# Kernel tuning notes

Hardware: AMD Instinct MI355X
Metric: run time of the kernel (lower is better)

The kernel has to match this reference:

```python
import jax, jax.numpy as jnp
import numpy as np

DIM = 1024
HEADS = 16
HEAD_DIM = DIM // HEADS
HIDDEN = 4 * DIM
EPS = 1e-5


def _layernorm(x, g, b):
    mu = jnp.mean(x, axis=-1, keepdims=True)
    var = jnp.mean(jnp.square(x - mu), axis=-1, keepdims=True)
    return (x - mu) * jax.lax.rsqrt(var + EPS) * g + b


def setup_inputs() -> dict:
    key = jax.random.key(0)
    ks = jax.random.split(key, 10)
    s = lambda fan_in: 1.0 / np.sqrt(fan_in)
    return {
        "x": jax.random.normal(ks[0], (8, 2048, DIM), dtype=jnp.float32),
        # weights stored (in, out): y = x @ W + b
        "w_qkv": jax.random.uniform(ks[1], (DIM, 3 * DIM), minval=-s(DIM), maxval=s(DIM)),
        "b_qkv": jnp.zeros((3 * DIM,), jnp.float32),
        "w_proj": jax.random.uniform(ks[2], (DIM, DIM), minval=-s(DIM), maxval=s(DIM)),
        "b_proj": jnp.zeros((DIM,), jnp.float32),
        "w_fc1": jax.random.uniform(ks[3], (DIM, HIDDEN), minval=-s(DIM), maxval=s(DIM)),
        "b_fc1": jnp.zeros((HIDDEN,), jnp.float32),
        "w_fc2": jax.random.uniform(ks[4], (HIDDEN, DIM), minval=-s(HIDDEN), maxval=s(HIDDEN)),
        "b_fc2": jnp.zeros((DIM,), jnp.float32),
        "g1": jnp.ones((DIM,), jnp.float32),
        "be1": jnp.zeros((DIM,), jnp.float32),
        "g2": jnp.ones((DIM,), jnp.float32),
        "be2": jnp.zeros((DIM,), jnp.float32),
    }


def reference(x, w_qkv, b_qkv, w_proj, b_proj, w_fc1, b_fc1, w_fc2, b_fc2, g1, be1, g2, be2):
    B, N, D = x.shape
    scale = HEAD_DIM ** -0.5

    # --- attention (faithful to source: q,k,v kept as (B,N,H,hd), no head permute) ---
    h = _layernorm(x, g1, be1)
    qkv = (h @ w_qkv + b_qkv).reshape(B, N, 3, HEADS, HEAD_DIM)
    q, k, v = qkv[:, :, 0], qkv[:, :, 1], qkv[:, :, 2]
    # (B,N,H,hd) @ (B,N,hd,H) -> per-token head-head scores (B,N,H,H)
    attn = jnp.einsum('bnhd,bngd->bnhg', q, k) * scale
    attn = jax.nn.softmax(attn, axis=-1)
    o = jnp.einsum('bnhg,bngd->bnhd', attn, v)          # (B,N,H,hd)
    o = jnp.transpose(o, (0, 2, 1, 3)).reshape(B, N, D)  # source's transpose(1,2).reshape
    x = x + o @ w_proj + b_proj

    # --- MLP ---
    h = _layernorm(x, g2, be2)
    h = jax.nn.gelu(h @ w_fc1 + b_fc1, approximate=False)  # torch nn.GELU default = exact
    x = x + h @ w_fc2 + b_fc2
    return x
```

## Files before the change

### kernel.cpp

```cpp
#include <hip/hip_runtime.h>
#include <hip/hip_bf16.h>
#include <math.h>

typedef unsigned short u16;
typedef __attribute__((ext_vector_type(8))) short bf16x8;
typedef __attribute__((ext_vector_type(4))) float f32x4;

#define NTOK 16384
#define LN_EPS 1e-5f

static __device__ __forceinline__ u16 f2bf(float f) {
  unsigned u = __float_as_uint(f);
  u += 0x7fffu + ((u >> 16) & 1u);
  return (u16)(u >> 16);
}
static __device__ __forceinline__ float bf2f(u16 u) {
  return __uint_as_float(((unsigned)u) << 16);
}

__global__ __launch_bounds__(256) void transpose_bf16(const float* __restrict__ in,
                                                      u16* __restrict__ out,
                                                      int K, int N) {
  __shared__ float tile[32][33];
  int n0 = blockIdx.x * 32, k0 = blockIdx.y * 32;
  int tx = threadIdx.x, ty = threadIdx.y;
#pragma unroll
  for (int i = 0; i < 32; i += 8)
    tile[ty + i][tx] = in[(size_t)(k0 + ty + i) * N + n0 + tx];
  __syncthreads();
#pragma unroll
  for (int i = 0; i < 32; i += 8)
    out[(size_t)(n0 + ty + i) * K + k0 + tx] = f2bf(tile[tx][ty + i]);
}

__global__ __launch_bounds__(256) void ln_bf16(const float* __restrict__ x,
                                               const float* __restrict__ g,
                                               const float* __restrict__ be,
                                               u16* __restrict__ out) {
  __shared__ float red[8];
  int row = blockIdx.x;
  int t = threadIdx.x;
  float4 v = ((const float4*)(x + (size_t)row * 1024))[t];
  float s = v.x + v.y + v.z + v.w;
  float ss = v.x * v.x + v.y * v.y + v.z * v.z + v.w * v.w;
#pragma unroll
  for (int i = 1; i < 64; i <<= 1) {
    s += __shfl_xor(s, i);
    ss += __shfl_xor(ss, i);
  }
  int lane = t & 63, wid = t >> 6;
  if (lane == 0) { red[wid] = s; red[4 + wid] = ss; }
  __syncthreads();
  s = red[0] + red[1] + red[2] + red[3];
  ss = red[4] + red[5] + red[6] + red[7];
  float mu = s * (1.0f / 1024.0f);
  float var = ss * (1.0f / 1024.0f) - mu * mu;
  float rs = rsqrtf(var + LN_EPS);
  float4 gv = ((const float4*)g)[t];
  float4 bv = ((const float4*)be)[t];
  ushort4 o;
  o.x = f2bf((v.x - mu) * rs * gv.x + bv.x);
  o.y = f2bf((v.y - mu) * rs * gv.y + bv.y);
  o.z = f2bf((v.z - mu) * rs * gv.z + bv.z);
  o.w = f2bf((v.w - mu) * rs * gv.w + bv.w);
  ((ushort4*)(out + (size_t)row * 1024))[t] = o;
}

__global__ __launch_bounds__(256) void attn_kernel(const u16* __restrict__ qkv,
                                                   u16* __restrict__ operm) {
  int tok = (blockIdx.x << 2) + (threadIdx.x >> 6);
  int lane = threadIdx.x & 63;
  int h = lane >> 2, sub = lane & 3;
  const u16* base = qkv + (size_t)tok * 3072;
  const u16* qp = base + h * 64;
  const u16* kp = base + 1024;
  const u16* vp = base + 2048;

  float sc[4] = {0.f, 0.f, 0.f, 0.f};
#pragma unroll
  for (int d0 = 0; d0 < 64; d0 += 8) {
    bf16x8 q8 = *(const bf16x8*)(qp + d0);
    float qf[8];
#pragma unroll
    for (int j = 0; j < 8; ++j) qf[j] = bf2f((u16)q8[j]);
#pragma unroll
    for (int gi = 0; gi < 4; ++gi) {
      bf16x8 k8 = *(const bf16x8*)(kp + (sub * 4 + gi) * 64 + d0);
#pragma unroll
      for (int j = 0; j < 8; ++j) sc[gi] += qf[j] * bf2f((u16)k8[j]);
    }
  }
  const float scale = 0.125f;
#pragma unroll
  for (int gi = 0; gi < 4; ++gi) sc[gi] *= scale;
  float mx = fmaxf(fmaxf(sc[0], sc[1]), fmaxf(sc[2], sc[3]));
  mx = fmaxf(mx, __shfl_xor(mx, 1));
  mx = fmaxf(mx, __shfl_xor(mx, 2));
  float p[4], sum = 0.f;
#pragma unroll
  for (int gi = 0; gi < 4; ++gi) { p[gi] = expf(sc[gi] - mx); sum += p[gi]; }
  sum += __shfl_xor(sum, 1);
  sum += __shfl_xor(sum, 2);
  float inv = 1.0f / sum;
#pragma unroll
  for (int gi = 0; gi < 4; ++gi) p[gi] *= inv;

  float pall[16];
#pragma unroll
  for (int g = 0; g < 16; ++g)
    pall[g] = __shfl(p[g & 3], (lane & ~3) | (g >> 2));

  float o[16];
#pragma unroll
  for (int j = 0; j < 16; ++j) o[j] = 0.f;
#pragma unroll
  for (int g = 0; g < 16; ++g) {
    bf16x8 v0 = *(const bf16x8*)(vp + g * 64 + sub * 16);
    bf16x8 v1 = *(const bf16x8*)(vp + g * 64 + sub * 16 + 8);
#pragma unroll
    for (int j = 0; j < 8; ++j) {
      o[j] += pall[g] * bf2f((u16)v0[j]);
      o[8 + j] += pall[g] * bf2f((u16)v1[j]);
    }
  }
  int b = tok >> 11, n = tok & 2047;
  size_t off = ((size_t)b << 21) + (size_t)(h * 128 + (n >> 4)) * 1024 +
               (size_t)((n & 15) * 64 + sub * 16);
  bf16x8 w0, w1;
#pragma unroll
  for (int j = 0; j < 8; ++j) {
    w0[j] = (short)f2bf(o[j]);
    w1[j] = (short)f2bf(o[8 + j]);
  }
  *(bf16x8*)(operm + off) = w0;
  *(bf16x8*)(operm + off + 8) = w1;
}

template <int EPI>
__global__ __launch_bounds__(512, 2) void gemm256(const u16* __restrict__ A,
                                                  const u16* __restrict__ BT,
                                                  const float* __restrict__ bias,
                                                  const float* __restrict__ res,
                                                  void* __restrict__ outp,
                                                  int M, int N, int K) {
  __shared__ u16 As[2][256 * 64];
  __shared__ u16 Bs[2][256 * 64];
  const int tid = threadIdx.x;
  const int wid = tid >> 6, lane = tid & 63;
  const int wm = wid >> 2, wn = wid & 3;
  const int lrow = lane & 15, lhi = lane >> 4;

  const int nbx = gridDim.x;
  const int nwg = nbx * gridDim.y;
  const int wg = blockIdx.y * nbx + blockIdx.x;
  const int cpx = nwg >> 3;
  const int swz = (wg & 7) * cpx + (wg >> 3);
  const int bn = swz % nbx, bm = swz / nbx;

  const int NT = K >> 6;

  const int r8 = tid >> 3;
  const int k8s = (tid & 7) ^ (r8 & 7);
  const u16* pA = A + (size_t)(bm * 256 + r8) * K + k8s * 8;
  const u16* pB = BT + (size_t)(bn * 256 + r8) * K + k8s * 8;
  const int ldsbase = wid * 512;

  auto stageAll = [&](int t) {
    if (t >= NT) return;
    const size_t koff = (size_t)t * 64;
    u16* la = &As[t & 1][0];
    u16* lb = &Bs[t & 1][0];
#pragma unroll
    for (int i = 0; i < 4; ++i) {
      __builtin_amdgcn_global_load_lds(
          (const __attribute__((address_space(1))) void*)(pA + koff + (size_t)i * 64 * K),
          (__attribute__((address_space(3))) void*)(la + i * 4096 + ldsbase), 16, 0, 0);
    }
#pragma unroll
    for (int i = 0; i < 4; ++i) {
      __builtin_amdgcn_global_load_lds(
          (const __attribute__((address_space(1))) void*)(pB + koff + (size_t)i * 64 * K),
          (__attribute__((address_space(3))) void*)(lb + i * 4096 + ldsbase), 16, 0, 0);
    }
  };

  stageAll(0);

  f32x4 acc[8][4] = {};
  const int rbA = wm * 128 + lrow;
  const int rbB = wn * 64 + lrow;
  const int swz8 = (lrow & 7);

  for (int t = 0; t < NT; ++t) {
    stageAll(t + 1);
    if (t + 1 < NT) {
      asm volatile("s_waitcnt vmcnt(8)" ::: "memory");
    } else {
      asm volatile("s_waitcnt vmcnt(0)" ::: "memory");
    }
    __builtin_amdgcn_s_barrier();
    __builtin_amdgcn_sched_barrier(0);

    const u16* Ab = &As[t & 1][0];
    const u16* Bb = &Bs[t & 1][0];
#pragma unroll
    for (int s = 0; s < 2; ++s) {
      const int sl = ((s * 4 + lhi) ^ swz8) << 3;
      bf16x8 bfv[4];
#pragma unroll
      for (int n = 0; n < 4; ++n)
        bfv[n] = *(const bf16x8*)(Bb + (rbB + n * 16) * 64 + sl);
#pragma unroll
      for (int q = 0; q < 4; ++q) {
        bf16x8 a0 = *(const bf16x8*)(Ab + (rbA + (2 * q) * 16) * 64 + sl);
        bf16x8 a1 = *(const bf16x8*)(Ab + (rbA + (2 * q + 1) * 16) * 64 + sl);
        __builtin_amdgcn_s_setprio(1);
#pragma unroll
        for (int n = 0; n < 4; ++n) {
          acc[2 * q][n] = __builtin_amdgcn_mfma_f32_16x16x32_bf16(a0, bfv[n], acc[2 * q][n], 0, 0, 0);
          acc[2 * q + 1][n] = __builtin_amdgcn_mfma_f32_16x16x32_bf16(a1, bfv[n], acc[2 * q + 1][n], 0, 0, 0);
        }
        __builtin_amdgcn_s_setprio(0);
      }
    }

    asm volatile("s_waitcnt lgkmcnt(0)" ::: "memory");
    __builtin_amdgcn_sched_barrier(0);
    __builtin_amdgcn_s_barrier();
    __builtin_amdgcn_sched_barrier(0);
  }

  const size_t crow0 = (size_t)bm * 256 + (size_t)wm * 128;
  const int ccol0 = bn * 256 + wn * 64;
#pragma unroll
  for (int n = 0; n < 4; ++n) {
    const int col = ccol0 + n * 16 + lrow;
    const float bb = bias[col];
#pragma unroll
    for (int m = 0; m < 8; ++m) {
#pragma unroll
      for (int r = 0; r < 4; ++r) {
        const size_t row = crow0 + m * 16 + lhi * 4 + r;
        const size_t idx = row * (size_t)N + col;
        float val = acc[m][n][r] + bb;
        if (EPI == 1 || EPI == 3) val += res[idx];
        if (EPI == 2) val = 0.5f * val * (1.0f + erff(val * 0.70710678118654752f));
        if (EPI == 0 || EPI == 2)
          ((u16*)outp)[idx] = f2bf(val);
        else
          ((float*)outp)[idx] = val;
      }
    }
  }
}

extern "C" void kernel_launch(void* const* d_in, const int* in_sizes, int n_in,
                              void* d_out, int out_size, void* d_ws, size_t ws_size,
                              hipStream_t stream) {
  const float* x = (const float*)d_in[0];
  const float* w_qkv = (const float*)d_in[1];
  const float* b_qkv = (const float*)d_in[2];
  const float* w_proj = (const float*)d_in[3];
  const float* b_proj = (const float*)d_in[4];
  const float* w_fc1 = (const float*)d_in[5];
  const float* b_fc1 = (const float*)d_in[6];
  const float* w_fc2 = (const float*)d_in[7];
  const float* b_fc2 = (const float*)d_in[8];
  const float* g1 = (const float*)d_in[9];
  const float* be1 = (const float*)d_in[10];
  const float* g2 = (const float*)d_in[11];
  const float* be2 = (const float*)d_in[12];
  float* out = (float*)d_out;

  char* ws = (char*)d_ws;
  u16* wqkvT = (u16*)ws; ws += (size_t)3072 * 1024 * 2;
  u16* wprojT = (u16*)ws; ws += (size_t)1024 * 1024 * 2;
  u16* wfc1T = (u16*)ws; ws += (size_t)4096 * 1024 * 2;
  u16* wfc2T = (u16*)ws; ws += (size_t)1024 * 4096 * 2;
  u16* hbuf = (u16*)ws; ws += (size_t)NTOK * 1024 * 2;
  u16* big = (u16*)ws;

  transpose_bf16<<<dim3(3072 / 32, 1024 / 32), dim3(32, 8), 0, stream>>>(w_qkv, wqkvT, 1024, 3072);
  transpose_bf16<<<dim3(1024 / 32, 1024 / 32), dim3(32, 8), 0, stream>>>(w_proj, wprojT, 1024, 1024);
  transpose_bf16<<<dim3(4096 / 32, 1024 / 32), dim3(32, 8), 0, stream>>>(w_fc1, wfc1T, 1024, 4096);
  transpose_bf16<<<dim3(1024 / 32, 4096 / 32), dim3(32, 8), 0, stream>>>(w_fc2, wfc2T, 4096, 1024);

  ln_bf16<<<NTOK, 256, 0, stream>>>(x, g1, be1, hbuf);

  gemm256<0><<<dim3(3072 / 256, NTOK / 256), 512, 0, stream>>>(hbuf, wqkvT, b_qkv, nullptr, big, NTOK, 3072, 1024);

  attn_kernel<<<NTOK / 4, 256, 0, stream>>>(big, hbuf);

  gemm256<1><<<dim3(1024 / 256, NTOK / 256), 512, 0, stream>>>(hbuf, wprojT, b_proj, x, out, NTOK, 1024, 1024);

  ln_bf16<<<NTOK, 256, 0, stream>>>(out, g2, be2, hbuf);

  gemm256<2><<<dim3(4096 / 256, NTOK / 256), 512, 0, stream>>>(hbuf, wfc1T, b_fc1, nullptr, big, NTOK, 4096, 1024);

  gemm256<3><<<dim3(1024 / 256, NTOK / 256), 512, 0, stream>>>(big, wfc2T, b_fc2, out, out, NTOK, 1024, 4096);
}
```

Baseline: 745.4 us.

## Interleave next-tile staging with MFMA phases and stage epilogue through LDS

The GEMM main loop is restructured so the next K-tile's A and B global-to-LDS loads are issued in separate quarter-phases of the MFMA work, with barriers between phases, instead of all at the top of each iteration. The epilogue now writes accumulators into a swizzled LDS buffer and then stores coalesced 16-byte vectors to global memory, with residual adds done on vectorized reads. The aim is to overlap memory traffic with compute and to replace strided scalar global stores with wide coalesced ones. In exchange the loop gains extra barriers per K-step and waits on vmcnt(0) at each iteration, and the epilogue adds LDS round-trips and extra syncs.

```diff
diff --git a/kernel.cpp b/kernel.cpp
--- a/kernel.cpp
+++ b/kernel.cpp
@@ -143,8 +143,9 @@
                                                   const float* __restrict__ res,
                                                   void* __restrict__ outp,
                                                   int M, int N, int K) {
-  __shared__ u16 As[2][256 * 64];
-  __shared__ u16 Bs[2][256 * 64];
+  __shared__ __align__(16) u16 SLDS[65536];
+  u16* As = SLDS;
+  u16* Bs = SLDS + 32768;
   const int tid = threadIdx.x;
   const int wid = tid >> 6, lane = tid & 63;
   const int wm = wid >> 2, wn = wid & 3;
@@ -165,90 +166,129 @@
   const u16* pB = BT + (size_t)(bn * 256 + r8) * K + k8s * 8;
   const int ldsbase = wid * 512;
 
-  auto stageAll = [&](int t) {
+  auto stageM = [&](const u16* p, u16* lb, int t) {
     if (t >= NT) return;
     const size_t koff = (size_t)t * 64;
-    u16* la = &As[t & 1][0];
-    u16* lb = &Bs[t & 1][0];
+    u16* l = lb + (t & 1) * 16384;
 #pragma unroll
     for (int i = 0; i < 4; ++i) {
       __builtin_amdgcn_global_load_lds(
-          (const __attribute__((address_space(1))) void*)(pA + koff + (size_t)i * 64 * K),
-          (__attribute__((address_space(3))) void*)(la + i * 4096 + ldsbase), 16, 0, 0);
-    }
-#pragma unroll
-    for (int i = 0; i < 4; ++i) {
-      __builtin_amdgcn_global_load_lds(
-          (const __attribute__((address_space(1))) void*)(pB + koff + (size_t)i * 64 * K),
-          (__attribute__((address_space(3))) void*)(lb + i * 4096 + ldsbase), 16, 0, 0);
+          (const __attribute__((address_space(1))) void*)(p + koff + (size_t)i * 64 * K),
+          (__attribute__((address_space(3))) void*)(l + i * 4096 + ldsbase), 16, 0, 0);
     }
   };
 
-  stageAll(0);
+  stageM(pA, As, 0);
+  stageM(pB, Bs, 0);
 
   f32x4 acc[8][4] = {};
   const int rbA = wm * 128 + lrow;
   const int rbB = wn * 64 + lrow;
-  const int swz8 = (lrow & 7);
+  const int swz8 = lrow & 7;
+  const int sl0 = ((0 + lhi) ^ swz8) << 3;
+  const int sl1 = ((4 + lhi) ^ swz8) << 3;
 
   for (int t = 0; t < NT; ++t) {
-    stageAll(t + 1);
-    if (t + 1 < NT) {
-      asm volatile("s_waitcnt vmcnt(8)" ::: "memory");
-    } else {
-      asm volatile("s_waitcnt vmcnt(0)" ::: "memory");
-    }
+    asm volatile("s_waitcnt vmcnt(0)" ::: "memory");
     __builtin_amdgcn_s_barrier();
-    __builtin_amdgcn_sched_barrier(0);
-
-    const u16* Ab = &As[t & 1][0];
-    const u16* Bb = &Bs[t & 1][0];
-#pragma unroll
-    for (int s = 0; s < 2; ++s) {
-      const int sl = ((s * 4 + lhi) ^ swz8) << 3;
-      bf16x8 bfv[4];
-#pragma unroll
-      for (int n = 0; n < 4; ++n)
-        bfv[n] = *(const bf16x8*)(Bb + (rbB + n * 16) * 64 + sl);
-#pragma unroll
-      for (int q = 0; q < 4; ++q) {
-        bf16x8 a0 = *(const bf16x8*)(Ab + (rbA + (2 * q) * 16) * 64 + sl);
-        bf16x8 a1 = *(const bf16x8*)(Ab + (rbA + (2 * q + 1) * 16) * 64 + sl);
-        __builtin_amdgcn_s_setprio(1);
+
+    const u16* Ab = As + (t & 1) * 16384;
+    const u16* Bb = Bs + (t & 1) * 16384;
+    bf16x8 bfv[4][2];
+#pragma unroll
+    for (int q = 0; q < 4; ++q) {
+      if (q == 0) {
 #pragma unroll
         for (int n = 0; n < 4; ++n) {
-          acc[2 * q][n] = __builtin_amdgcn_mfma_f32_16x16x32_bf16(a0, bfv[n], acc[2 * q][n], 0, 0, 0);
-          acc[2 * q + 1][n] = __builtin_amdgcn_mfma_f32_16x16x32_bf16(a1, bfv[n], acc[2 * q + 1][n], 0, 0, 0);
+          bfv[n][0] = *(const bf16x8*)(Bb + (rbB + n * 16) * 64 + sl0);
+          bfv[n][1] = *(const bf16x8*)(Bb + (rbB + n * 16) * 64 + sl1);
         }
-        __builtin_amdgcn_s_setprio(0);
-      }
-    }
-
-    asm volatile("s_waitcnt lgkmcnt(0)" ::: "memory");
-    __builtin_amdgcn_sched_barrier(0);
-    __builtin_amdgcn_s_barrier();
-    __builtin_amdgcn_sched_barrier(0);
-  }
-
-  const size_t crow0 = (size_t)bm * 256 + (size_t)wm * 128;
-  const int ccol0 = bn * 256 + wn * 64;
-#pragma unroll
-  for (int n = 0; n < 4; ++n) {
-    const int col = ccol0 + n * 16 + lrow;
-    const float bb = bias[col];
-#pragma unroll
-    for (int m = 0; m < 8; ++m) {
-#pragma unroll
-      for (int r = 0; r < 4; ++r) {
-        const size_t row = crow0 + m * 16 + lhi * 4 + r;
-        const size_t idx = row * (size_t)N + col;
-        float val = acc[m][n][r] + bb;
-        if (EPI == 1 || EPI == 3) val += res[idx];
-        if (EPI == 2) val = 0.5f * val * (1.0f + erff(val * 0.70710678118654752f));
-        if (EPI == 0 || EPI == 2)
-          ((u16*)outp)[idx] = f2bf(val);
-        else
-          ((float*)outp)[idx] = val;
+      }
+      bf16x8 af[2][2];
+#pragma unroll
+      for (int j = 0; j < 2; ++j) {
+        const int row = rbA + (2 * q + j) * 16;
+        af[j][0] = *(const bf16x8*)(Ab + row * 64 + sl0);
+        af[j][1] = *(const bf16x8*)(Ab + row * 64 + sl1);
+      }
+      if (q == 0) stageM(pA, As, t + 1);
+      if (q == 1) stageM(pB, Bs, t + 1);
+      __builtin_amdgcn_s_barrier();
+      asm volatile("s_waitcnt lgkmcnt(0)" ::: "memory");
+      __builtin_amdgcn_sched_barrier(0);
+      __builtin_amdgcn_s_setprio(1);
+#pragma unroll
+      for (int j = 0; j < 2; ++j)
+#pragma unroll
+        for (int n = 0; n < 4; ++n) {
+          acc[2 * q + j][n] = __builtin_amdgcn_mfma_f32_16x16x32_bf16(af[j][0], bfv[n][0], acc[2 * q + j][n], 0, 0, 0);
+          acc[2 * q + j][n] = __builtin_amdgcn_mfma_f32_16x16x32_bf16(af[j][1], bfv[n][1], acc[2 * q + j][n], 0, 0, 0);
+        }
+      __builtin_amdgcn_s_setprio(0);
+      __builtin_amdgcn_s_barrier();
+    }
+  }
+
+  __syncthreads();
+  const int crow0 = bm * 256;
+  const int ccol0 = bn * 256;
+
+  if (EPI == 0 || EPI == 2) {
+    u16* Cl = SLDS;
+#pragma unroll
+    for (int n = 0; n < 4; ++n) {
+      const int col = wn * 64 + n * 16 + lrow;
+      const float bb = bias[ccol0 + col];
+#pragma unroll
+      for (int m = 0; m < 8; ++m) {
+#pragma unroll
+        for (int r = 0; r < 4; ++r) {
+          const int row = wm * 128 + m * 16 + lhi * 4 + r;
+          float val = acc[m][n][r] + bb;
+          if (EPI == 2) val = 0.5f * val * (1.0f + erff(val * 0.70710678118654752f));
+          Cl[row * 256 + (col ^ ((row & 12) << 2))] = f2bf(val);
+        }
+      }
+    }
+    __syncthreads();
+    const int rl = tid >> 5, ch = tid & 31;
+#pragma unroll
+    for (int it = 0; it < 16; ++it) {
+      const int row = it * 16 + rl;
+      const int pch = ch ^ (((row >> 2) & 3) << 1);
+      bf16x8 v = *(const bf16x8*)(Cl + row * 256 + pch * 8);
+      *(bf16x8*)((u16*)outp + (size_t)(crow0 + row) * N + ccol0 + ch * 8) = v;
+    }
+  } else {
+    float* Cf = (float*)SLDS;
+#pragma unroll
+    for (int h = 0; h < 2; ++h) {
+      if (h) __syncthreads();
+      if (wm == h) {
+#pragma unroll
+        for (int n = 0; n < 4; ++n) {
+          const int col = wn * 64 + n * 16 + lrow;
+          const float bb = bias[ccol0 + col];
+#pragma unroll
+          for (int m = 0; m < 8; ++m)
+#pragma unroll
+            for (int r = 0; r < 4; ++r) {
+              const int row = m * 16 + lhi * 4 + r;
+              Cf[row * 256 + (col ^ ((row & 4) << 2))] = acc[m][n][r] + bb;
+            }
+        }
+      }
+      __syncthreads();
+      const int rl = tid >> 6, ch = tid & 63;
+#pragma unroll
+      for (int it = 0; it < 16; ++it) {
+        const int row = it * 8 + rl;
+        const int pch = ch ^ (((row >> 2) & 1) << 2);
+        f32x4 v = *(const f32x4*)(Cf + row * 256 + pch * 4);
+        const size_t gidx = (size_t)(crow0 + h * 128 + row) * N + ccol0 + ch * 4;
+        const f32x4 rv = *(const f32x4*)(res + gidx);
+        v = v + rv;
+        *(f32x4*)((float*)outp + gidx) = v;
       }
     }
   }
```

Result: faster. 625.6 us (-16.1%).
